# Kernel tuning notes

Hardware: AMD Instinct MI355X
Metric: run time of the kernel (lower is better)

## Reference

```python
import jax, jax.numpy as jnp
import numpy as np

B, N, M = 256, 2048, 128          # batch, memory rows, memory word size
VEC, H, E = 256, 1024, 512        # vector_length, hidden_size, embed_dim
SHIFTS = 3                        # shift kernel size {-1,0,+1}
P = M + 3 + SHIFTS                # k(M), beta(1), g(1), s(3), gamma(1)
EPS = 1e-16


def _xavier(k, shape):
    fan_out, fan_in = shape
    lim = float(np.sqrt(6.0 / (fan_in + fan_out)))
    return jax.random.uniform(k, shape, jnp.float32, -lim, lim)


def setup_inputs() -> dict:
    key = jax.random.key(0)
    ks = jax.random.split(key, 16)
    x = jax.random.normal(ks[0], (B, VEC + M), jnp.float32)
    memory = jax.random.normal(ks[1], (B, N, M), jnp.float32) * 0.1
    prev_read_w = jax.nn.softmax(jax.random.normal(ks[2], (B, N), jnp.float32), axis=1)
    prev_write_w = jax.nn.softmax(jax.random.normal(ks[3], (B, N), jnp.float32), axis=1)
    h_prev = jax.random.normal(ks[4], (B, H), jnp.float32) * 0.1
    c_prev = jax.random.normal(ks[5], (B, H), jnp.float32) * 0.1
    # LSTM controller params (torch gate order i,f,g,o)
    W_ih = _xavier(ks[6], (4 * H, VEC + M))
    W_hh = _xavier(ks[7], (4 * H, H))
    b_ih = jnp.zeros((4 * H,), jnp.float32)
    b_hh = jnp.zeros((4 * H,), jnp.float32)
    # read head fc: hidden -> k,beta,g,s,gamma
    W_r = _xavier(ks[8], (P, H)); b_r = jnp.zeros((P,), jnp.float32)
    # write head fc: hidden -> k,beta,g,s,gamma,e(M),a(M)
    W_w = _xavier(ks[9], (P + 2 * M, H)); b_w = jnp.zeros((P + 2 * M,), jnp.float32)
    # output fc: (hidden + M) -> embed_dim
    W_fc = _xavier(ks[10], (E, H + M))
    b_fc = jax.random.normal(ks[11], (E,), jnp.float32) * 0.01
    return dict(x=x, memory=memory, prev_read_w=prev_read_w, prev_write_w=prev_write_w,
                h_prev=h_prev, c_prev=c_prev, W_ih=W_ih, W_hh=W_hh, b_ih=b_ih, b_hh=b_hh,
                W_r=W_r, b_r=b_r, W_w=W_w, b_w=b_w, W_fc=W_fc, b_fc=b_fc)


def _address(p, memory, prev_w):
    # p: [B, P] raw head parameters; memory: [B,N,M]; prev_w: [B,N]
    k = jnp.tanh(p[:, :M])                                   # [B,M]
    beta = jax.nn.softplus(p[:, M:M + 1])                    # [B,1]
    g = jax.nn.sigmoid(p[:, M + 1:M + 2])                    # [B,1]
    s = jax.nn.softmax(p[:, M + 2:M + 2 + SHIFTS], axis=1)   # [B,3]
    gamma = 1.0 + jax.nn.softplus(p[:, M + 2 + SHIFTS:P])    # [B,1]
    # content addressing: cosine similarity * beta -> softmax over N
    dot = jnp.einsum('bnm,bm->bn', memory, k)
    denom = jnp.linalg.norm(memory, axis=-1) * jnp.linalg.norm(k, axis=-1, keepdims=True) + EPS
    w_c = jax.nn.softmax(beta * (dot / denom), axis=1)
    # gated interpolation with previous weights
    w_g = g * w_c + (1.0 - g) * prev_w
    # circular convolution with 3-tap shift kernel
    w_t = (s[:, 0:1] * jnp.roll(w_g, 1, axis=1)
           + s[:, 1:2] * w_g
           + s[:, 2:3] * jnp.roll(w_g, -1, axis=1))
    # sharpening
    w_p = w_t ** gamma
    return w_p / (jnp.sum(w_p, axis=1, keepdims=True) + EPS)


def reference(x, memory, prev_read_w, prev_write_w, h_prev, c_prev,
              W_ih, W_hh, b_ih, b_hh, W_r, b_r, W_w, b_w, W_fc, b_fc):
    # LSTM controller step
    gates = x @ W_ih.T + b_ih + h_prev @ W_hh.T + b_hh
    i, f, gg, o = jnp.split(gates, 4, axis=1)
    c = jax.nn.sigmoid(f) * c_prev + jax.nn.sigmoid(i) * jnp.tanh(gg)
    h = jax.nn.sigmoid(o) * jnp.tanh(c)                       # controller output [B,H]
    # read head: address then read
    w_r = _address(h @ W_r.T + b_r, memory, prev_read_w)
    read = jnp.einsum('bn,bnm->bm', w_r, memory)              # [B,M]
    # write head: address then erase/add
    wp = h @ W_w.T + b_w
    w_w = _address(wp[:, :P], memory, prev_write_w)
    e = jax.nn.sigmoid(wp[:, P:P + M])                        # erase [B,M]
    a = jnp.tanh(wp[:, P + M:P + 2 * M])                      # add   [B,M]
    new_memory = memory * (1.0 - w_w[:, :, None] * e[:, None, :]) + w_w[:, :, None] * a[:, None, :]
    # output
    out = jax.nn.sigmoid(jnp.concatenate([h, read], axis=1) @ W_fc.T + b_fc)  # [B,E]
    return out, new_memory
```

## Files before the change

kernel.cpp:

```cpp
#include <hip/hip_runtime.h>
#include <hip/hip_bf16.h>

#define B_    256
#define N_    2048
#define M_    128
#define VEC_  256
#define H_    1024
#define E_    512
#define P_    134
#define XDIM  384
#define G4H   4096
#define PWC   524

typedef float  floatx4  __attribute__((ext_vector_type(4)));
typedef short  bf16x8   __attribute__((ext_vector_type(8)));
typedef unsigned short ushortx8 __attribute__((ext_vector_type(8)));
typedef unsigned short ushortx4 __attribute__((ext_vector_type(4)));

#define OFF_GATES 0
#define OFF_H     (OFF_GATES + B_*G4H)
#define OFF_PW    (OFF_H     + B_*H_)
#define OFF_KR    (OFF_PW    + B_*PWC)
#define OFF_KW    (OFF_KR    + B_*M_)
#define OFF_E     (OFF_KW    + B_*M_)
#define OFF_A     (OFF_E     + B_*M_)
#define OFF_SCAL  (OFF_A     + B_*M_)
#define OFF_DOTR  (OFF_SCAL  + B_*16)
#define OFF_DOTW  (OFF_DOTR  + B_*N_)
#define OFF_MNORM (OFF_DOTW  + B_*N_)
#define OFF_WR    (OFF_MNORM + B_*N_)
#define OFF_WW    (OFF_WR    + B_*N_)
#define OFF_READ  (OFF_WW    + B_*N_)
#define FLOAT_TOTAL (OFF_READ + B_*M_)
#define SOFF_X    0
#define SOFF_H    (SOFF_X   + B_*XDIM)
#define SOFF_WIH  (SOFF_H   + B_*H_)
#define SOFF_WHH  (SOFF_WIH + G4H*XDIM)
#define SHORT_TOTAL (SOFF_WHH + G4H*H_)

__device__ __forceinline__ float bf2f(unsigned short u) {
    return __uint_as_float(((unsigned int)u) << 16);
}
__device__ __forceinline__ unsigned short f2bf(float f) {
    unsigned int x = __float_as_uint(f);
    x += 0x7fffu + ((x >> 16) & 1u);
    return (unsigned short)(x >> 16);
}
__device__ __forceinline__ float sigm(float x) { return 1.f / (1.f + expf(-x)); }
__device__ __forceinline__ float softplus_(float x) { return x > 20.f ? x : log1pf(expf(x)); }

__global__ __launch_bounds__(256) void k_cvt4(
    const float* __restrict__ s0, const float* __restrict__ s1,
    const float* __restrict__ s2, const float* __restrict__ s3,
    unsigned short* __restrict__ dst)
{
    int i = (blockIdx.x * 256 + threadIdx.x) * 4;
    const float* s; int off;
    if      (i < SOFF_H)    { s = s0; off = SOFF_X; }
    else if (i < SOFF_WIH)  { s = s1; off = SOFF_H; }
    else if (i < SOFF_WHH)  { s = s2; off = SOFF_WIH; }
    else                    { s = s3; off = SOFF_WHH; }
    floatx4 v = *(const floatx4*)(s + (i - off));
    ushortx4 o;
    o[0] = f2bf(v[0]); o[1] = f2bf(v[1]); o[2] = f2bf(v[2]); o[3] = f2bf(v[3]);
    *(ushortx4*)(dst + i) = o;
}

__global__ __launch_bounds__(256) void k_gates(
    const unsigned short* __restrict__ wsb,
    const float* __restrict__ b_ih, const float* __restrict__ b_hh,
    float* __restrict__ gates)
{
    const unsigned short* x      = wsb + SOFF_X;
    const unsigned short* h_prev = wsb + SOFF_H;
    const unsigned short* W_ih   = wsb + SOFF_WIH;
    const unsigned short* W_hh   = wsb + SOFF_WHH;

    int gtid  = blockIdx.x * 256 + threadIdx.x;
    int wid   = gtid >> 6;
    int lane  = threadIdx.x & 63;
    int tileM = wid >> 6;
    int nGrp  = wid & 63;
    int m0 = tileM << 4, n0 = nGrp << 6;
    int quad = lane >> 4, r16 = lane & 15;
    int koff = quad << 3;
    int mA = m0 + r16;

    floatx4 acc[4];
#pragma unroll
    for (int s = 0; s < 4; ++s) acc[s] = (floatx4){0.f, 0.f, 0.f, 0.f};

    const unsigned short* xrow = x + mA * XDIM;
    const unsigned short* hrow = h_prev + mA * H_;

#pragma unroll 2
    for (int kk = 0; kk < 12; ++kk) {
        int k = (kk << 5) + koff;
        bf16x8 a  = *(const bf16x8*)(xrow + k);
        bf16x8 b0 = *(const bf16x8*)(W_ih + (n0 +  0 + r16) * XDIM + k);
        bf16x8 b1 = *(const bf16x8*)(W_ih + (n0 + 16 + r16) * XDIM + k);
        bf16x8 b2 = *(const bf16x8*)(W_ih + (n0 + 32 + r16) * XDIM + k);
        bf16x8 b3 = *(const bf16x8*)(W_ih + (n0 + 48 + r16) * XDIM + k);
        acc[0] = __builtin_amdgcn_mfma_f32_16x16x32_bf16(a, b0, acc[0], 0, 0, 0);
        acc[1] = __builtin_amdgcn_mfma_f32_16x16x32_bf16(a, b1, acc[1], 0, 0, 0);
        acc[2] = __builtin_amdgcn_mfma_f32_16x16x32_bf16(a, b2, acc[2], 0, 0, 0);
        acc[3] = __builtin_amdgcn_mfma_f32_16x16x32_bf16(a, b3, acc[3], 0, 0, 0);
    }
#pragma unroll 2
    for (int kk = 0; kk < 32; ++kk) {
        int k = (kk << 5) + koff;
        bf16x8 a  = *(const bf16x8*)(hrow + k);
        bf16x8 b0 = *(const bf16x8*)(W_hh + (n0 +  0 + r16) * H_ + k);
        bf16x8 b1 = *(const bf16x8*)(W_hh + (n0 + 16 + r16) * H_ + k);
        bf16x8 b2 = *(const bf16x8*)(W_hh + (n0 + 32 + r16) * H_ + k);
        bf16x8 b3 = *(const bf16x8*)(W_hh + (n0 + 48 + r16) * H_ + k);
        acc[0] = __builtin_amdgcn_mfma_f32_16x16x32_bf16(a, b0, acc[0], 0, 0, 0);
        acc[1] = __builtin_amdgcn_mfma_f32_16x16x32_bf16(a, b1, acc[1], 0, 0, 0);
        acc[2] = __builtin_amdgcn_mfma_f32_16x16x32_bf16(a, b2, acc[2], 0, 0, 0);
        acc[3] = __builtin_amdgcn_mfma_f32_16x16x32_bf16(a, b3, acc[3], 0, 0, 0);
    }
#pragma unroll
    for (int s = 0; s < 4; ++s) {
        int n = n0 + (s << 4) + r16;
        float bias = b_ih[n] + b_hh[n];
#pragma unroll
        for (int r = 0; r < 4; ++r) {
            int m = m0 + (quad << 2) + r;
            gates[m * G4H + n] = acc[s][r] + bias;
        }
    }
}

__global__ __launch_bounds__(256) void k_lstm(
    const float* __restrict__ gates, const float* __restrict__ c_prev,
    float* __restrict__ h)
{
    int idx = blockIdx.x * 256 + threadIdx.x;
    int b = idx >> 10, j = idx & 1023;
    const float* g = gates + b * G4H;
    float ig = sigm(g[j]);
    float fg = sigm(g[1024 + j]);
    float gg = tanhf(g[2048 + j]);
    float og = sigm(g[3072 + j]);
    float c  = fg * c_prev[idx] + ig * gg;
    h[idx] = og * tanhf(c);
}

__global__ __launch_bounds__(256) void k_heads(
    const float* __restrict__ h,
    const float* __restrict__ W_r, const float* __restrict__ b_r,
    const float* __restrict__ W_w, const float* __restrict__ b_w,
    float* __restrict__ pw)
{
    __shared__ float hs[H_];
    int b = blockIdx.x, t = threadIdx.x;
    for (int i = t; i < H_; i += 256) hs[i] = h[b * H_ + i];
    __syncthreads();
    for (int c = t; c < PWC; c += 256) {
        const float* wrow;
        float bias;
        if (c < P_) { wrow = W_r + c * H_;             bias = b_r[c]; }
        else        { int j = c - P_; wrow = W_w + j * H_; bias = b_w[j]; }
        float acc = 0.f;
#pragma unroll 4
        for (int k = 0; k < H_; k += 4) {
            floatx4 wv = *(const floatx4*)(wrow + k);
            acc = fmaf(wv[0], hs[k], acc);
            acc = fmaf(wv[1], hs[k + 1], acc);
            acc = fmaf(wv[2], hs[k + 2], acc);
            acc = fmaf(wv[3], hs[k + 3], acc);
        }
        pw[b * PWC + c] = acc + bias;
    }
}

__global__ __launch_bounds__(128) void k_params(
    const float* __restrict__ pw,
    float* __restrict__ kr, float* __restrict__ kw,
    float* __restrict__ e,  float* __restrict__ a,
    float* __restrict__ scal, float* __restrict__ read_acc)
{
    int b = blockIdx.x, t = threadIdx.x;
    const float* p = pw + b * PWC;
    float krv = tanhf(p[t]);
    float kwv = tanhf(p[P_ + t]);
    kr[b * M_ + t] = krv;
    kw[b * M_ + t] = kwv;
    e [b * M_ + t] = sigm (p[268 + t]);
    a [b * M_ + t] = tanhf(p[396 + t]);
    read_acc[b * M_ + t] = 0.f;

    float sr = krv * krv, sw = kwv * kwv;
#pragma unroll
    for (int m = 32; m; m >>= 1) { sr += __shfl_xor(sr, m); sw += __shfl_xor(sw, m); }
    __shared__ float red[4];
    if ((t & 63) == 0) { red[(t >> 6) * 2] = sr; red[(t >> 6) * 2 + 1] = sw; }
    __syncthreads();
    if (t == 0) {
        float nr = sqrtf(red[0] + red[2]);
        float nw = sqrtf(red[1] + red[3]);
        float* sc = scal + b * 16;
        {
            float beta = softplus_(p[128]);
            float g    = sigm(p[129]);
            float s0 = p[130], s1 = p[131], s2 = p[132];
            float mx = fmaxf(s0, fmaxf(s1, s2));
            float e0 = expf(s0 - mx), e1 = expf(s1 - mx), e2 = expf(s2 - mx);
            float es = e0 + e1 + e2;
            sc[0] = beta; sc[1] = g; sc[2] = e0 / es; sc[3] = e1 / es; sc[4] = e2 / es;
            sc[5] = 1.f + softplus_(p[133]); sc[6] = nr;
        }
        {
            float beta = softplus_(p[262]);
            float g    = sigm(p[263]);
            float s0 = p[264], s1 = p[265], s2 = p[266];
            float mx = fmaxf(s0, fmaxf(s1, s2));
            float e0 = expf(s0 - mx), e1 = expf(s1 - mx), e2 = expf(s2 - mx);
            float es = e0 + e1 + e2;
            sc[8] = beta; sc[9] = g; sc[10] = e0 / es; sc[11] = e1 / es; sc[12] = e2 / es;
            sc[13] = 1.f + softplus_(p[267]); sc[14] = nw;
        }
    }
}

__global__ __launch_bounds__(256) void k_pass1(
    const float* __restrict__ memory,
    const float* __restrict__ kr, const float* __restrict__ kw,
    float* __restrict__ dotr, float* __restrict__ dotw, float* __restrict__ mnorm)
{
    int b = blockIdx.x >> 4;
    int chunk = blockIdx.x & 15;
    __shared__ float krs[M_], kws[M_];
    int t = threadIdx.x;
    if (t < 128) krs[t] = kr[b * M_ + t];
    else         kws[t - 128] = kw[b * M_ + t - 128];
    __syncthreads();
    int wave = t >> 6, lane = t & 63;
    float k0r = krs[lane * 2], k1r = krs[lane * 2 + 1];
    float k0w = kws[lane * 2], k1w = kws[lane * 2 + 1];
    for (int i = 0; i < 32; ++i) {
        int n = chunk * 128 + wave * 32 + i;
        size_t ro = (size_t)b * N_ + n;
        float2 mv = *(const float2*)(memory + ro * M_ + lane * 2);
        float m0 = mv.x, m1 = mv.y;
        float dr = m0 * k0r + m1 * k1r;
        float dw = m0 * k0w + m1 * k1w;
        float ss = m0 * m0 + m1 * m1;
#pragma unroll
        for (int m = 32; m; m >>= 1) {
            dr += __shfl_xor(dr, m);
            dw += __shfl_xor(dw, m);
            ss += __shfl_xor(ss, m);
        }
        if (lane == 0) {
            dotr[ro] = dr; dotw[ro] = dw; mnorm[ro] = sqrtf(ss);
        }
    }
}

__device__ __forceinline__ float blkSum(float v, float* red) {
#pragma unroll
    for (int m = 32; m; m >>= 1) v += __shfl_xor(v, m);
    int w = threadIdx.x >> 6;
    if ((threadIdx.x & 63) == 0) red[w] = v;
    __syncthreads();
    float r = red[0] + red[1] + red[2] + red[3];
    __syncthreads();
    return r;
}
__device__ __forceinline__ float blkMax(float v, float* red) {
#pragma unroll
    for (int m = 32; m; m >>= 1) v = fmaxf(v, __shfl_xor(v, m));
    int w = threadIdx.x >> 6;
    if ((threadIdx.x & 63) == 0) red[w] = v;
    __syncthreads();
    float r = fmaxf(fmaxf(red[0], red[1]), fmaxf(red[2], red[3]));
    __syncthreads();
    return r;
}

__global__ __launch_bounds__(256) void k_address(
    const float* __restrict__ dotr, const float* __restrict__ dotw,
    const float* __restrict__ mnorm,
    const float* __restrict__ prev_r, const float* __restrict__ prev_w,
    const float* __restrict__ scal,
    float* __restrict__ wr, float* __restrict__ ww)
{
    int b = blockIdx.x >> 1, head = blockIdx.x & 1;
    const float* dot = head ? dotw : dotr;
    const float* prev = head ? prev_w : prev_r;
    float* wout = head ? ww : wr;
    const float* sc = scal + b * 16 + head * 8;
    float beta = sc[0], g = sc[1], s0 = sc[2], s1 = sc[3], s2 = sc[4];
    float gamma = sc[5], kn = sc[6];

    __shared__ float buf[N_];
    __shared__ float red[4];
    int t = threadIdx.x;
    size_t base = (size_t)b * N_;

    float loc[8];
    float mx = -1e30f;
#pragma unroll
    for (int i = 0; i < 8; ++i) {
        int n = (i << 8) + t;
        float xv = beta * dot[base + n] / (mnorm[base + n] * kn + 1e-16f);
        loc[i] = xv;
        mx = fmaxf(mx, xv);
    }
    mx = blkMax(mx, red);
    float sum = 0.f;
#pragma unroll
    for (int i = 0; i < 8; ++i) { float ev = expf(loc[i] - mx); loc[i] = ev; sum += ev; }
    sum = blkSum(sum, red);
    float inv = 1.f / sum;
#pragma unroll
    for (int i = 0; i < 8; ++i) {
        int n = (i << 8) + t;
        float wc = loc[i] * inv;
        buf[n] = g * wc + (1.f - g) * prev[base + n];
    }
    __syncthreads();
    float psum = 0.f;
#pragma unroll
    for (int i = 0; i < 8; ++i) {
        int n = (i << 8) + t;
        float wt = s0 * buf[(n + N_ - 1) & (N_ - 1)] + s1 * buf[n] + s2 * buf[(n + 1) & (N_ - 1)];
        float wp = powf(wt, gamma);
        loc[i] = wp;
        psum += wp;
    }
    psum = blkSum(psum, red);
    float invp = 1.f / (psum + 1e-16f);
#pragma unroll
    for (int i = 0; i < 8; ++i) {
        int n = (i << 8) + t;
        wout[base + n] = loc[i] * invp;
    }
}

__global__ __launch_bounds__(256) void k_update(
    const float* __restrict__ memory,
    const float* __restrict__ wr, const float* __restrict__ ww,
    const float* __restrict__ e, const float* __restrict__ a,
    float* __restrict__ read_acc,
    float* __restrict__ newmem)
{
    int b = blockIdx.x >> 6;
    int chunk = blockIdx.x & 63;
    int t = threadIdx.x;
    __shared__ float es[M_], as_[M_];
    if (t < 128) es[t] = e[b * M_ + t];
    else         as_[t - 128] = a[b * M_ + t - 128];
    __syncthreads();

    int c = t & 15, r = t >> 4;
    int m8 = c << 3;
    float ev[8], av[8], racc[8];
#pragma unroll
    for (int j = 0; j < 8; ++j) { ev[j] = es[m8 + j]; av[j] = as_[m8 + j]; racc[j] = 0.f; }

#pragma unroll
    for (int stp = 0; stp < 2; ++stp) {
        int n = chunk * 32 + stp * 16 + r;
        size_t ro = (size_t)b * N_ + n;
        floatx4 mv0 = *(const floatx4*)(memory + ro * M_ + m8);
        floatx4 mv1 = *(const floatx4*)(memory + ro * M_ + m8 + 4);
        float wwv = ww[ro], wrv = wr[ro];
        floatx4 o0, o1;
#pragma unroll
        for (int j = 0; j < 4; ++j) {
            float mf = mv0[j];
            o0[j] = mf * (1.f - wwv * ev[j]) + wwv * av[j];
            racc[j] = fmaf(wrv, mf, racc[j]);
        }
#pragma unroll
        for (int j = 0; j < 4; ++j) {
            float mf = mv1[j];
            o1[j] = mf * (1.f - wwv * ev[4 + j]) + wwv * av[4 + j];
            racc[4 + j] = fmaf(wrv, mf, racc[4 + j]);
        }
        *(floatx4*)(newmem + ro * M_ + m8) = o0;
        *(floatx4*)(newmem + ro * M_ + m8 + 4) = o1;
    }

    __shared__ float rbuf[16][M_];
#pragma unroll
    for (int j = 0; j < 8; ++j) rbuf[r][m8 + j] = racc[j];
    __syncthreads();
    if (t < 128) {
        float s = 0.f;
#pragma unroll
        for (int rr = 0; rr < 16; ++rr) s += rbuf[rr][t];
        atomicAdd(read_acc + b * M_ + t, s);
    }
}

__global__ __launch_bounds__(256) void k_out(
    const float* __restrict__ h, const float* __restrict__ read_acc,
    const float* __restrict__ W_fc, const float* __restrict__ b_fc,
    float* __restrict__ out)
{
    __shared__ float hc[H_ + M_];
    int b = blockIdx.x, t = threadIdx.x;
    for (int i = t; i < H_; i += 256) hc[i] = h[b * H_ + i];
    if (t < 128) hc[H_ + t] = read_acc[b * M_ + t];
    __syncthreads();
#pragma unroll
    for (int cc = 0; cc < 2; ++cc) {
        int c = cc * 256 + t;
        const float* wrow = W_fc + c * (H_ + M_);
        float acc = 0.f;
#pragma unroll 4
        for (int k = 0; k < H_ + M_; k += 4) {
            floatx4 wv = *(const floatx4*)(wrow + k);
            acc = fmaf(wv[0], hc[k], acc);
            acc = fmaf(wv[1], hc[k + 1], acc);
            acc = fmaf(wv[2], hc[k + 2], acc);
            acc = fmaf(wv[3], hc[k + 3], acc);
        }
        acc += b_fc[c];
        out[b * E_ + c] = sigm(acc);
    }
}

extern "C" void kernel_launch(void* const* d_in, const int* in_sizes, int n_in,
                              void* d_out, int out_size, void* d_ws, size_t ws_size,
                              hipStream_t stream)
{
    (void)in_sizes; (void)n_in; (void)out_size; (void)ws_size;
    const float* x      = (const float*)d_in[0];
    const float* memory = (const float*)d_in[1];
    const float* prev_r = (const float*)d_in[2];
    const float* prev_w = (const float*)d_in[3];
    const float* h_prev = (const float*)d_in[4];
    const float* c_prev = (const float*)d_in[5];
    const float* W_ih   = (const float*)d_in[6];
    const float* W_hh   = (const float*)d_in[7];
    const float* b_ih   = (const float*)d_in[8];
    const float* b_hh   = (const float*)d_in[9];
    const float* W_r    = (const float*)d_in[10];
    const float* b_r    = (const float*)d_in[11];
    const float* W_w    = (const float*)d_in[12];
    const float* b_w    = (const float*)d_in[13];
    const float* W_fc   = (const float*)d_in[14];
    const float* b_fc   = (const float*)d_in[15];

    float* ws = (float*)d_ws;
    float* gates = ws + OFF_GATES;
    float* h     = ws + OFF_H;
    float* pw    = ws + OFF_PW;
    float* kr    = ws + OFF_KR;
    float* kw    = ws + OFF_KW;
    float* e     = ws + OFF_E;
    float* a     = ws + OFF_A;
    float* scal  = ws + OFF_SCAL;
    float* dotr  = ws + OFF_DOTR;
    float* dotw  = ws + OFF_DOTW;
    float* mnorm = ws + OFF_MNORM;
    float* wrb   = ws + OFF_WR;
    float* wwb   = ws + OFF_WW;
    float* rd    = ws + OFF_READ;
    unsigned short* wsb = (unsigned short*)(ws + FLOAT_TOTAL);

    float* out    = (float*)d_out;
    float* newmem = out + B_ * E_;

    k_cvt4   <<<SHORT_TOTAL / 1024, 256, 0, stream>>>(x, h_prev, W_ih, W_hh, wsb);
    k_gates  <<<256,   256, 0, stream>>>(wsb, b_ih, b_hh, gates);
    k_lstm   <<<1024,  256, 0, stream>>>(gates, c_prev, h);
    k_heads  <<<256,   256, 0, stream>>>(h, W_r, b_r, W_w, b_w, pw);
    k_params <<<256,   128, 0, stream>>>(pw, kr, kw, e, a, scal, rd);
    k_pass1  <<<4096,  256, 0, stream>>>(memory, kr, kw, dotr, dotw, mnorm);
    k_address<<<512,   256, 0, stream>>>(dotr, dotw, mnorm, prev_r, prev_w, scal, wrb, wwb);
    k_update <<<16384, 256, 0, stream>>>(memory, wrb, wwb, e, a, rd, newmem);
    k_out    <<<256,   256, 0, stream>>>(h, rd, W_fc, b_fc, out);
}
```

Measured before the change: 778.3 us.

## Fuse LSTM, head projections and param activation; retile gates GEMM; nontemporal memory streaming

Merges the LSTM cell, read/write head projection and head-parameter activation kernels into one per-batch kernel that keeps h and the projections in shared memory, removing two launches and global round trips. The gates GEMM moves to 32-column tiles with twice the blocks. The memory passes now use float4 nontemporal loads and stores, and each update block covers 64 rows. The output projection computes two columns per thread with vectorised shared reads.

```diff
diff --git a/kernel.cpp b/kernel.cpp
--- a/kernel.cpp
+++ b/kernel.cpp
@@ -79,48 +79,40 @@
     int gtid  = blockIdx.x * 256 + threadIdx.x;
     int wid   = gtid >> 6;
     int lane  = threadIdx.x & 63;
-    int tileM = wid >> 6;
-    int nGrp  = wid & 63;
-    int m0 = tileM << 4, n0 = nGrp << 6;
+    int tileM = wid >> 7;
+    int nGrp  = wid & 127;
+    int m0 = tileM << 4, n0 = nGrp << 5;
     int quad = lane >> 4, r16 = lane & 15;
     int koff = quad << 3;
     int mA = m0 + r16;
 
-    floatx4 acc[4];
-#pragma unroll
-    for (int s = 0; s < 4; ++s) acc[s] = (floatx4){0.f, 0.f, 0.f, 0.f};
+    floatx4 acc[2];
+#pragma unroll
+    for (int s = 0; s < 2; ++s) acc[s] = (floatx4){0.f, 0.f, 0.f, 0.f};
 
     const unsigned short* xrow = x + mA * XDIM;
     const unsigned short* hrow = h_prev + mA * H_;
 
-#pragma unroll 2
+#pragma unroll 4
     for (int kk = 0; kk < 12; ++kk) {
         int k = (kk << 5) + koff;
         bf16x8 a  = *(const bf16x8*)(xrow + k);
         bf16x8 b0 = *(const bf16x8*)(W_ih + (n0 +  0 + r16) * XDIM + k);
         bf16x8 b1 = *(const bf16x8*)(W_ih + (n0 + 16 + r16) * XDIM + k);
-        bf16x8 b2 = *(const bf16x8*)(W_ih + (n0 + 32 + r16) * XDIM + k);
-        bf16x8 b3 = *(const bf16x8*)(W_ih + (n0 + 48 + r16) * XDIM + k);
         acc[0] = __builtin_amdgcn_mfma_f32_16x16x32_bf16(a, b0, acc[0], 0, 0, 0);
         acc[1] = __builtin_amdgcn_mfma_f32_16x16x32_bf16(a, b1, acc[1], 0, 0, 0);
-        acc[2] = __builtin_amdgcn_mfma_f32_16x16x32_bf16(a, b2, acc[2], 0, 0, 0);
-        acc[3] = __builtin_amdgcn_mfma_f32_16x16x32_bf16(a, b3, acc[3], 0, 0, 0);
-    }
-#pragma unroll 2
+    }
+#pragma unroll 4
     for (int kk = 0; kk < 32; ++kk) {
         int k = (kk << 5) + koff;
         bf16x8 a  = *(const bf16x8*)(hrow + k);
         bf16x8 b0 = *(const bf16x8*)(W_hh + (n0 +  0 + r16) * H_ + k);
         bf16x8 b1 = *(const bf16x8*)(W_hh + (n0 + 16 + r16) * H_ + k);
-        bf16x8 b2 = *(const bf16x8*)(W_hh + (n0 + 32 + r16) * H_ + k);
-        bf16x8 b3 = *(const bf16x8*)(W_hh + (n0 + 48 + r16) * H_ + k);
         acc[0] = __builtin_amdgcn_mfma_f32_16x16x32_bf16(a, b0, acc[0], 0, 0, 0);
         acc[1] = __builtin_amdgcn_mfma_f32_16x16x32_bf16(a, b1, acc[1], 0, 0, 0);
-        acc[2] = __builtin_amdgcn_mfma_f32_16x16x32_bf16(a, b2, acc[2], 0, 0, 0);
-        acc[3] = __builtin_amdgcn_mfma_f32_16x16x32_bf16(a, b3, acc[3], 0, 0, 0);
-    }
-#pragma unroll
-    for (int s = 0; s < 4; ++s) {
+    }
+#pragma unroll
+    for (int s = 0; s < 2; ++s) {
         int n = n0 + (s << 4) + r16;
         float bias = b_ih[n] + b_hh[n];
 #pragma unroll
@@ -131,94 +123,99 @@
     }
 }
 
-__global__ __launch_bounds__(256) void k_lstm(
+__global__ __launch_bounds__(256) void k_ctrl(
     const float* __restrict__ gates, const float* __restrict__ c_prev,
-    float* __restrict__ h)
-{
-    int idx = blockIdx.x * 256 + threadIdx.x;
-    int b = idx >> 10, j = idx & 1023;
-    const float* g = gates + b * G4H;
-    float ig = sigm(g[j]);
-    float fg = sigm(g[1024 + j]);
-    float gg = tanhf(g[2048 + j]);
-    float og = sigm(g[3072 + j]);
-    float c  = fg * c_prev[idx] + ig * gg;
-    h[idx] = og * tanhf(c);
-}
-
-__global__ __launch_bounds__(256) void k_heads(
-    const float* __restrict__ h,
     const float* __restrict__ W_r, const float* __restrict__ b_r,
     const float* __restrict__ W_w, const float* __restrict__ b_w,
-    float* __restrict__ pw)
-{
-    __shared__ float hs[H_];
-    int b = blockIdx.x, t = threadIdx.x;
-    for (int i = t; i < H_; i += 256) hs[i] = h[b * H_ + i];
-    __syncthreads();
-    for (int c = t; c < PWC; c += 256) {
-        const float* wrow;
-        float bias;
-        if (c < P_) { wrow = W_r + c * H_;             bias = b_r[c]; }
-        else        { int j = c - P_; wrow = W_w + j * H_; bias = b_w[j]; }
-        float acc = 0.f;
-#pragma unroll 4
-        for (int k = 0; k < H_; k += 4) {
-            floatx4 wv = *(const floatx4*)(wrow + k);
-            acc = fmaf(wv[0], hs[k], acc);
-            acc = fmaf(wv[1], hs[k + 1], acc);
-            acc = fmaf(wv[2], hs[k + 2], acc);
-            acc = fmaf(wv[3], hs[k + 3], acc);
-        }
-        pw[b * PWC + c] = acc + bias;
-    }
-}
-
-__global__ __launch_bounds__(128) void k_params(
-    const float* __restrict__ pw,
+    float* __restrict__ h_out,
     float* __restrict__ kr, float* __restrict__ kw,
     float* __restrict__ e,  float* __restrict__ a,
     float* __restrict__ scal, float* __restrict__ read_acc)
 {
+    __shared__ __align__(16) float hs[H_];
+    __shared__ __align__(16) float pws[PWC];
+    __shared__ float red[8];
     int b = blockIdx.x, t = threadIdx.x;
-    const float* p = pw + b * PWC;
-    float krv = tanhf(p[t]);
-    float kwv = tanhf(p[P_ + t]);
-    kr[b * M_ + t] = krv;
-    kw[b * M_ + t] = kwv;
-    e [b * M_ + t] = sigm (p[268 + t]);
-    a [b * M_ + t] = tanhf(p[396 + t]);
-    read_acc[b * M_ + t] = 0.f;
-
+    const float* g = gates + (size_t)b * G4H;
+
+#pragma unroll
+    for (int jj = 0; jj < 4; ++jj) {
+        int j = t + (jj << 8);
+        float ig = sigm(g[j]);
+        float fg = sigm(g[1024 + j]);
+        float gg = tanhf(g[2048 + j]);
+        float og = sigm(g[3072 + j]);
+        float c  = fg * c_prev[b * H_ + j] + ig * gg;
+        float hv = og * tanhf(c);
+        hs[j] = hv;
+        h_out[b * H_ + j] = hv;
+    }
+    __syncthreads();
+
+    int c0 = t, c1 = t + 256, c2v = (t < 12);
+    const float* w0; float bias0;
+    if (c0 < P_) { w0 = W_r + c0 * H_; bias0 = b_r[c0]; }
+    else         { w0 = W_w + (c0 - P_) * H_; bias0 = b_w[c0 - P_]; }
+    const float* w1 = W_w + (c1 - P_) * H_;
+    float bias1 = b_w[c1 - P_];
+    const float* w2 = W_w + (c2v ? (t + 512 - P_) : 0) * H_;
+    float acc0 = 0.f, acc1 = 0.f, acc2 = 0.f;
+#pragma unroll 4
+    for (int k = 0; k < H_; k += 4) {
+        floatx4 hv = *(const floatx4*)&hs[k];
+        floatx4 a0 = *(const floatx4*)(w0 + k);
+        floatx4 a1 = *(const floatx4*)(w1 + k);
+        floatx4 a2 = *(const floatx4*)(w2 + k);
+#pragma unroll
+        for (int j = 0; j < 4; ++j) {
+            acc0 = fmaf(a0[j], hv[j], acc0);
+            acc1 = fmaf(a1[j], hv[j], acc1);
+            acc2 = fmaf(a2[j], hv[j], acc2);
+        }
+    }
+    pws[c0] = acc0 + bias0;
+    pws[c1] = acc1 + bias1;
+    if (c2v) pws[t + 512] = acc2 + b_w[t + 512 - P_];
+    __syncthreads();
+
+    float krv = 0.f, kwv = 0.f;
+    if (t < 128) {
+        krv = tanhf(pws[t]);
+        kwv = tanhf(pws[P_ + t]);
+        kr[b * M_ + t] = krv;
+        kw[b * M_ + t] = kwv;
+        e [b * M_ + t] = sigm (pws[268 + t]);
+        a [b * M_ + t] = tanhf(pws[396 + t]);
+        read_acc[b * M_ + t] = 0.f;
+    }
     float sr = krv * krv, sw = kwv * kwv;
 #pragma unroll
     for (int m = 32; m; m >>= 1) { sr += __shfl_xor(sr, m); sw += __shfl_xor(sw, m); }
-    __shared__ float red[4];
     if ((t & 63) == 0) { red[(t >> 6) * 2] = sr; red[(t >> 6) * 2 + 1] = sw; }
     __syncthreads();
     if (t == 0) {
-        float nr = sqrtf(red[0] + red[2]);
-        float nw = sqrtf(red[1] + red[3]);
+        float nr = sqrtf(red[0] + red[2] + red[4] + red[6]);
+        float nw = sqrtf(red[1] + red[3] + red[5] + red[7]);
         float* sc = scal + b * 16;
         {
-            float beta = softplus_(p[128]);
-            float g    = sigm(p[129]);
-            float s0 = p[130], s1 = p[131], s2 = p[132];
+            float beta = softplus_(pws[128]);
+            float gg   = sigm(pws[129]);
+            float s0 = pws[130], s1 = pws[131], s2 = pws[132];
             float mx = fmaxf(s0, fmaxf(s1, s2));
             float e0 = expf(s0 - mx), e1 = expf(s1 - mx), e2 = expf(s2 - mx);
             float es = e0 + e1 + e2;
-            sc[0] = beta; sc[1] = g; sc[2] = e0 / es; sc[3] = e1 / es; sc[4] = e2 / es;
-            sc[5] = 1.f + softplus_(p[133]); sc[6] = nr;
+            sc[0] = beta; sc[1] = gg; sc[2] = e0 / es; sc[3] = e1 / es; sc[4] = e2 / es;
+            sc[5] = 1.f + softplus_(pws[133]); sc[6] = nr;
         }
         {
-            float beta = softplus_(p[262]);
-            float g    = sigm(p[263]);
-            float s0 = p[264], s1 = p[265], s2 = p[266];
+            float beta = softplus_(pws[262]);
+            float gg   = sigm(pws[263]);
+            float s0 = pws[264], s1 = pws[265], s2 = pws[266];
             float mx = fmaxf(s0, fmaxf(s1, s2));
             float e0 = expf(s0 - mx), e1 = expf(s1 - mx), e2 = expf(s2 - mx);
             float es = e0 + e1 + e2;
-            sc[8] = beta; sc[9] = g; sc[10] = e0 / es; sc[11] = e1 / es; sc[12] = e2 / es;
-            sc[13] = 1.f + softplus_(p[267]); sc[14] = nw;
+            sc[8] = beta; sc[9] = gg; sc[10] = e0 / es; sc[11] = e1 / es; sc[12] = e2 / es;
+            sc[13] = 1.f + softplus_(pws[267]); sc[14] = nw;
         }
     }
 }
@@ -230,29 +227,32 @@
 {
     int b = blockIdx.x >> 4;
     int chunk = blockIdx.x & 15;
-    __shared__ float krs[M_], kws[M_];
+    __shared__ __align__(16) float krs[M_], kws[M_];
     int t = threadIdx.x;
     if (t < 128) krs[t] = kr[b * M_ + t];
     else         kws[t - 128] = kw[b * M_ + t - 128];
     __syncthreads();
     int wave = t >> 6, lane = t & 63;
-    float k0r = krs[lane * 2], k1r = krs[lane * 2 + 1];
-    float k0w = kws[lane * 2], k1w = kws[lane * 2 + 1];
-    for (int i = 0; i < 32; ++i) {
-        int n = chunk * 128 + wave * 32 + i;
+    int col  = (lane & 31) << 2;
+    int half = lane >> 5;
+    floatx4 kr4 = *(const floatx4*)&krs[col];
+    floatx4 kw4 = *(const floatx4*)&kws[col];
+    int rowbase = chunk * 128 + wave * 32;
+#pragma unroll 4
+    for (int i = 0; i < 16; ++i) {
+        int n = rowbase + (i << 1) + half;
         size_t ro = (size_t)b * N_ + n;
-        float2 mv = *(const float2*)(memory + ro * M_ + lane * 2);
-        float m0 = mv.x, m1 = mv.y;
-        float dr = m0 * k0r + m1 * k1r;
-        float dw = m0 * k0w + m1 * k1w;
-        float ss = m0 * m0 + m1 * m1;
-#pragma unroll
-        for (int m = 32; m; m >>= 1) {
+        floatx4 mv = __builtin_nontemporal_load((const floatx4*)(memory + ro * M_ + col));
+        float dr = mv[0] * kr4[0] + mv[1] * kr4[1] + mv[2] * kr4[2] + mv[3] * kr4[3];
+        float dw = mv[0] * kw4[0] + mv[1] * kw4[1] + mv[2] * kw4[2] + mv[3] * kw4[3];
+        float ss = mv[0] * mv[0] + mv[1] * mv[1] + mv[2] * mv[2] + mv[3] * mv[3];
+#pragma unroll
+        for (int m = 16; m; m >>= 1) {
             dr += __shfl_xor(dr, m);
             dw += __shfl_xor(dw, m);
             ss += __shfl_xor(ss, m);
         }
-        if (lane == 0) {
+        if ((lane & 31) == 0) {
             dotr[ro] = dr; dotw[ro] = dw; mnorm[ro] = sqrtf(ss);
         }
     }
@@ -346,8 +346,8 @@
     float* __restrict__ read_acc,
     float* __restrict__ newmem)
 {
-    int b = blockIdx.x >> 6;
-    int chunk = blockIdx.x & 63;
+    int b = blockIdx.x >> 5;
+    int chunk = blockIdx.x & 31;
     int t = threadIdx.x;
     __shared__ float es[M_], as_[M_];
     if (t < 128) es[t] = e[b * M_ + t];
@@ -361,11 +361,11 @@
     for (int j = 0; j < 8; ++j) { ev[j] = es[m8 + j]; av[j] = as_[m8 + j]; racc[j] = 0.f; }
 
 #pragma unroll
-    for (int stp = 0; stp < 2; ++stp) {
-        int n = chunk * 32 + stp * 16 + r;
+    for (int stp = 0; stp < 4; ++stp) {
+        int n = chunk * 64 + stp * 16 + r;
         size_t ro = (size_t)b * N_ + n;
-        floatx4 mv0 = *(const floatx4*)(memory + ro * M_ + m8);
-        floatx4 mv1 = *(const floatx4*)(memory + ro * M_ + m8 + 4);
+        floatx4 mv0 = __builtin_nontemporal_load((const floatx4*)(memory + ro * M_ + m8));
+        floatx4 mv1 = __builtin_nontemporal_load((const floatx4*)(memory + ro * M_ + m8 + 4));
         float wwv = ww[ro], wrv = wr[ro];
         floatx4 o0, o1;
 #pragma unroll
@@ -380,8 +380,8 @@
             o1[j] = mf * (1.f - wwv * ev[4 + j]) + wwv * av[4 + j];
             racc[4 + j] = fmaf(wrv, mf, racc[4 + j]);
         }
-        *(floatx4*)(newmem + ro * M_ + m8) = o0;
-        *(floatx4*)(newmem + ro * M_ + m8 + 4) = o1;
+        __builtin_nontemporal_store(o0, (floatx4*)(newmem + ro * M_ + m8));
+        __builtin_nontemporal_store(o1, (floatx4*)(newmem + ro * M_ + m8 + 4));
     }
 
     __shared__ float rbuf[16][M_];
@@ -401,27 +401,28 @@
     const float* __restrict__ W_fc, const float* __restrict__ b_fc,
     float* __restrict__ out)
 {
-    __shared__ float hc[H_ + M_];
+    __shared__ __align__(16) float hc[H_ + M_];
     int b = blockIdx.x, t = threadIdx.x;
     for (int i = t; i < H_; i += 256) hc[i] = h[b * H_ + i];
     if (t < 128) hc[H_ + t] = read_acc[b * M_ + t];
     __syncthreads();
-#pragma unroll
-    for (int cc = 0; cc < 2; ++cc) {
-        int c = cc * 256 + t;
-        const float* wrow = W_fc + c * (H_ + M_);
-        float acc = 0.f;
+    int c0 = t, c1 = t + 256;
+    const float* w0 = W_fc + c0 * (H_ + M_);
+    const float* w1 = W_fc + c1 * (H_ + M_);
+    float acc0 = 0.f, acc1 = 0.f;
 #pragma unroll 4
-        for (int k = 0; k < H_ + M_; k += 4) {
-            floatx4 wv = *(const floatx4*)(wrow + k);
-            acc = fmaf(wv[0], hc[k], acc);
-            acc = fmaf(wv[1], hc[k + 1], acc);
-            acc = fmaf(wv[2], hc[k + 2], acc);
-            acc = fmaf(wv[3], hc[k + 3], acc);
-        }
-        acc += b_fc[c];
-        out[b * E_ + c] = sigm(acc);
-    }
+    for (int k = 0; k < H_ + M_; k += 4) {
+        floatx4 hv = *(const floatx4*)&hc[k];
+        floatx4 a0 = *(const floatx4*)(w0 + k);
+        floatx4 a1 = *(const floatx4*)(w1 + k);
+#pragma unroll
+        for (int j = 0; j < 4; ++j) {
+            acc0 = fmaf(a0[j], hv[j], acc0);
+            acc1 = fmaf(a1[j], hv[j], acc1);
+        }
+    }
+    out[b * E_ + c0] = sigm(acc0 + b_fc[c0]);
+    out[b * E_ + c1] = sigm(acc1 + b_fc[c1]);
 }
 
 extern "C" void kernel_launch(void* const* d_in, const int* in_sizes, int n_in,
@@ -449,7 +450,6 @@
     float* ws = (float*)d_ws;
     float* gates = ws + OFF_GATES;
     float* h     = ws + OFF_H;
-    float* pw    = ws + OFF_PW;
     float* kr    = ws + OFF_KR;
     float* kw    = ws + OFF_KW;
     float* e     = ws + OFF_E;
@@ -467,12 +467,11 @@
     float* newmem = out + B_ * E_;
 
     k_cvt4   <<<SHORT_TOTAL / 1024, 256, 0, stream>>>(x, h_prev, W_ih, W_hh, wsb);
-    k_gates  <<<256,   256, 0, stream>>>(wsb, b_ih, b_hh, gates);
-    k_lstm   <<<1024,  256, 0, stream>>>(gates, c_prev, h);
-    k_heads  <<<256,   256, 0, stream>>>(h, W_r, b_r, W_w, b_w, pw);
-    k_params <<<256,   128, 0, stream>>>(pw, kr, kw, e, a, scal, rd);
+    k_gates  <<<512,   256, 0, stream>>>(wsb, b_ih, b_hh, gates);
+    k_ctrl   <<<256,   256, 0, stream>>>(gates, c_prev, W_r, b_r, W_w, b_w,
+                                         h, kr, kw, e, a, scal, rd);
     k_pass1  <<<4096,  256, 0, stream>>>(memory, kr, kw, dotr, dotw, mnorm);
     k_address<<<512,   256, 0, stream>>>(dotr, dotw, mnorm, prev_r, prev_w, scal, wrb, wwb);
-    k_update <<<16384, 256, 0, stream>>>(memory, wrb, wwb, e, a, rd, newmem);
+    k_update <<<8192,  256, 0, stream>>>(memory, wrb, wwb, e, a, rd, newmem);
     k_out    <<<256,   256, 0, stream>>>(h, rd, W_fc, b_fc, out);
 }
```

Measured after the change: 771.4 us. Within noise of the previous version (-0.9%).
